# Kernel optimization log

Hardware: AMD Instinct MI355X
Metric: run time of the kernel (lower is better)

The kernel has to match this reference:

```python
import jax, jax.numpy as jnp
import numpy as np
import math

B, T, D, H = 4, 2048, 1024, 16
HD = D // H  # 64

def setup_inputs() -> dict:
    key = jax.random.key(0)
    ks = jax.random.split(key, 11)
    s = 1.0 / math.sqrt(D)
    return {
        "q": jax.random.normal(ks[0], (B, T, D), jnp.float32),
        "k": jax.random.normal(ks[1], (B, T, D), jnp.float32),
        "v": jax.random.normal(ks[2], (B, T, D), jnp.float32),
        "Wq": jax.random.normal(ks[3], (D, D), jnp.float32) * s,
        "bq": jnp.zeros((D,), jnp.float32),
        "Wk": jax.random.normal(ks[4], (D, D), jnp.float32) * s,
        "bk": jnp.zeros((D,), jnp.float32),
        "Wv": jax.random.normal(ks[5], (D, D), jnp.float32) * s,
        "bv": jnp.zeros((D,), jnp.float32),
        "Wo": jax.random.normal(ks[6], (D, D), jnp.float32) * s,
        "bo": jnp.zeros((D,), jnp.float32),
    }

def reference(q, k, v, Wq, bq, Wk, bk, Wv, bv, Wo, bo):
    # Linear projections (torch Linear: x @ W.T + b)
    qp = q @ Wq.T + bq
    kp = k @ Wk.T + bk
    vp = v @ Wv.T + bv
    # [B, T, D] -> [B, H, T, HD]
    def split(x):
        return x.reshape(B, T, H, HD).transpose(0, 2, 1, 3)
    qh, kh, vh = split(qp), split(kp), split(vp)
    # scaled dot-product attention
    score = jnp.einsum('bhqd,bhkd->bhqk', qh, kh) / math.sqrt(HD)
    attn = jax.nn.softmax(score, axis=-1)
    out = jnp.einsum('bhqk,bhkd->bhqd', attn, vh)
    # merge heads and output projection
    out = out.transpose(0, 2, 1, 3).reshape(B, T, D)
    return out @ Wo.T + bo
```

## Files before the change

kernel.cpp:

```cpp
#include <hip/hip_runtime.h>
#include <hip/hip_bf16.h>
#include <stdint.h>

#define B_ 4
#define T_ 2048
#define D_ 1024
#define H_ 16
#define HD_ 64
#define NKT (T_ / 64)

typedef __bf16 bf16;
typedef __bf16 bf16x8 __attribute__((ext_vector_type(8)));
typedef __bf16 bf16x4 __attribute__((ext_vector_type(4)));
typedef float f32x4 __attribute__((ext_vector_type(4)));
typedef uint32_t u32x4 __attribute__((ext_vector_type(4)));

#define QSCALE 0.18033688011112042f

__device__ __forceinline__ float fast_exp2(float x) {
#if __has_builtin(__builtin_amdgcn_exp2f)
    return __builtin_amdgcn_exp2f(x);
#else
    return exp2f(x);
#endif
}

__device__ __forceinline__ void async_load16(const bf16* g, const bf16* lds_uniform) {
    __builtin_amdgcn_global_load_lds(
        (const __attribute__((address_space(1))) uint32_t*)(uintptr_t)g,
        (__attribute__((address_space(3))) uint32_t*)(uintptr_t)lds_uniform,
        16, 0, 0);
}

__device__ __forceinline__ uint32_t pack2_bf16(float lo, float hi) {
    union { uint32_t u; __bf16 h[2]; } r;
    r.h[0] = (__bf16)lo;
    r.h[1] = (__bf16)hi;
    return r.u;
}

__device__ __forceinline__ void permswap16(uint32_t& a, uint32_t& b) {
    asm("v_permlane16_swap_b32 %0, %1" : "+v"(a), "+v"(b));
}

__global__ __launch_bounds__(256) void cast3(const float* __restrict__ s0, bf16* __restrict__ d0,
                                             const float* __restrict__ s1, bf16* __restrict__ d1,
                                             const float* __restrict__ s2, bf16* __restrict__ d2,
                                             int n4) {
    const float* s = blockIdx.y == 0 ? s0 : (blockIdx.y == 1 ? s1 : s2);
    bf16* d = blockIdx.y == 0 ? d0 : (blockIdx.y == 1 ? d1 : d2);
    int i = blockIdx.x * 256 + threadIdx.x;
    if (i < n4) {
        f32x4 v = ((const f32x4*)s)[i];
        bf16x4 o;
        o.x = (bf16)v.x; o.y = (bf16)v.y; o.z = (bf16)v.z; o.w = (bf16)v.w;
        ((bf16x4*)d)[i] = o;
    }
}

__global__ __launch_bounds__(256) void cast4(const float* __restrict__ s0, bf16* __restrict__ d0,
                                             const float* __restrict__ s1, bf16* __restrict__ d1,
                                             const float* __restrict__ s2, bf16* __restrict__ d2,
                                             const float* __restrict__ s3, bf16* __restrict__ d3,
                                             int n4) {
    const float* s = blockIdx.y == 0 ? s0 : (blockIdx.y == 1 ? s1 : (blockIdx.y == 2 ? s2 : s3));
    bf16* d = blockIdx.y == 0 ? d0 : (blockIdx.y == 1 ? d1 : (blockIdx.y == 2 ? d2 : d3));
    int i = blockIdx.x * 256 + threadIdx.x;
    if (i < n4) {
        f32x4 v = ((const f32x4*)s)[i];
        bf16x4 o;
        o.x = (bf16)v.x; o.y = (bf16)v.y; o.z = (bf16)v.z; o.w = (bf16)v.w;
        ((bf16x4*)d)[i] = o;
    }
}

template <typename OutT, int VMODE>
__device__ __forceinline__ void gemm_body(const bf16* __restrict__ A,
                                          const bf16* __restrict__ W,
                                          const float* __restrict__ bias,
                                          OutT* __restrict__ C,
                                          int lin, float scale,
                                          bf16* As, bf16* Bs, bf16* Tt) {
    const int K = D_, N = D_;
    const int tid = threadIdx.x;
    const int wid = tid >> 6, lane = tid & 63;
    const int quad = lane >> 4, l15 = lane & 15;
    const int wm = (wid >> 1) * 64, wn = (wid & 1) * 64;
    const int bx = N >> 7;
    const int ty = (lin & 7) + 8 * (lin / (8 * bx));
    const int tx = (lin >> 3) % bx;
    const long rowA0 = (long)ty * 128;
    const long rowB0 = (long)tx * 128;
    const int srow = lane >> 2;
    const int schunk = (lane & 3) * 8;
    const int sbase = (wid * 32) * 32;

    f32x4 acc[4][4];
#pragma unroll
    for (int i = 0; i < 4; i++)
#pragma unroll
        for (int j = 0; j < 4; j++) acc[i][j] = (f32x4){0.f, 0.f, 0.f, 0.f};

#pragma unroll
    for (int s = 0; s < 2; s++) {
        int r = wid * 32 + s * 16 + srow;
        async_load16(&A[(rowA0 + r) * K + schunk], &As[sbase + s * 16 * 32]);
        async_load16(&W[(rowB0 + r) * K + schunk], &Bs[sbase + s * 16 * 32]);
    }
    __syncthreads();

    const int NIT = K >> 5;
    for (int it = 0; it < NIT; it++) {
        const int cur = it & 1;
        const int co = cur * (128 * 32);
        if (it + 1 < NIT) {
            const int k1 = (it + 1) << 5;
            const int no = (cur ^ 1) * (128 * 32);
#pragma unroll
            for (int s = 0; s < 2; s++) {
                int r = wid * 32 + s * 16 + srow;
                async_load16(&A[(rowA0 + r) * K + k1 + schunk], &As[no + sbase + s * 16 * 32]);
                async_load16(&W[(rowB0 + r) * K + k1 + schunk], &Bs[no + sbase + s * 16 * 32]);
            }
        }
        bf16x8 af[4], bfr[4];
#pragma unroll
        for (int i = 0; i < 4; i++)
            af[i] = *(const bf16x8*)&As[co + (wm + i * 16 + l15) * 32 + quad * 8];
#pragma unroll
        for (int j = 0; j < 4; j++)
            bfr[j] = *(const bf16x8*)&Bs[co + (wn + j * 16 + l15) * 32 + quad * 8];
#pragma unroll
        for (int i = 0; i < 4; i++)
#pragma unroll
            for (int j = 0; j < 4; j++)
                acc[i][j] = __builtin_amdgcn_mfma_f32_16x16x32_bf16(af[i], bfr[j],
                                                                    acc[i][j], 0, 0, 0);
        __syncthreads();
    }

    if constexpr (VMODE == 0) {
#pragma unroll
        for (int i = 0; i < 4; i++) {
            long m = rowA0 + wm + i * 16 + quad * 4;
#pragma unroll
            for (int j = 0; j < 4; j++) {
                long n = rowB0 + wn + j * 16 + l15;
                float bb = bias[n];
#pragma unroll
                for (int r = 0; r < 4; r++) {
                    float v = (acc[i][j][r] + bb) * scale;
                    C[(m + r) * N + n] = (OutT)v;
                }
            }
        }
    } else {
#pragma unroll
        for (int i = 0; i < 4; i++) {
            int ml = wm + i * 16 + quad * 4;
#pragma unroll
            for (int j = 0; j < 4; j++) {
                int nl = wn + j * 16 + l15;
                float bb = bias[rowB0 + nl];
                bf16x4 ov = {(bf16)(acc[i][j][0] + bb), (bf16)(acc[i][j][1] + bb),
                             (bf16)(acc[i][j][2] + bb), (bf16)(acc[i][j][3] + bb)};
                *(bf16x4*)&Tt[nl * 136 + ml] = ov;
            }
        }
        __syncthreads();
        const long bidx = rowA0 >> 11;
        const int t0 = (int)(rowA0 & 2047);
#pragma unroll
        for (int p = 0; p < 8; p++) {
            int nl = p * 16 + (tid >> 4);
            int c = tid & 15;
            bf16x8 val = *(const bf16x8*)&Tt[nl * 136 + c * 8];
            int n = (int)rowB0 + nl;
            long vrow = (bidx * H_ + (n >> 6)) * (long)HD_ + (n & 63);
            int cp = (c & ~3) | ((c & 1) << 1) | ((c & 2) >> 1);
            *(bf16x8*)&((bf16*)C)[vrow * T_ + t0 + cp * 8] = val;
        }
    }
}

__global__ __launch_bounds__(256) void gemm_qkv(const bf16* __restrict__ Xq,
                                                const bf16* __restrict__ WqB,
                                                const float* __restrict__ bq,
                                                bf16* __restrict__ Qp,
                                                const bf16* __restrict__ Xk,
                                                const bf16* __restrict__ WkB,
                                                const float* __restrict__ bk,
                                                bf16* __restrict__ Kp,
                                                const bf16* __restrict__ Xv,
                                                const bf16* __restrict__ WvB,
                                                const float* __restrict__ bv,
                                                bf16* __restrict__ VtG) {
    __shared__ __align__(16) char sm[34816];
    bf16* As = (bf16*)sm;
    bf16* Bs = (bf16*)(sm + 16384);
    bf16* Tt = (bf16*)sm;
    const int p = blockIdx.x >> 9;
    const int lin = blockIdx.x & 511;
    if (p == 0)
        gemm_body<bf16, 0>(Xq, WqB, bq, Qp, lin, QSCALE, As, Bs, Tt);
    else if (p == 1)
        gemm_body<bf16, 0>(Xk, WkB, bk, Kp, lin, 1.f, As, Bs, Tt);
    else
        gemm_body<bf16, 1>(Xv, WvB, bv, VtG, lin, 1.f, As, Bs, Tt);
}

__global__ __launch_bounds__(256) void gemm_out(const bf16* __restrict__ Op,
                                                const bf16* __restrict__ WoB,
                                                const float* __restrict__ bo,
                                                float* __restrict__ out) {
    __shared__ __align__(16) char sm[32768];
    bf16* As = (bf16*)sm;
    bf16* Bs = (bf16*)(sm + 16384);
    gemm_body<float, 0>(Op, WoB, bo, out, blockIdx.x, 1.f, As, Bs, nullptr);
}

__global__ __launch_bounds__(512, 8) void attn_kernel(const bf16* __restrict__ Qp,
                                                      const bf16* __restrict__ Kp,
                                                      const bf16* __restrict__ VT,
                                                      bf16* __restrict__ Op) {
    __shared__ bf16 smem[4][64 * 64];
    const int tid = threadIdx.x;
    const int wid = tid >> 6, lane = tid & 63;
    const int quad = lane >> 4, l15 = lane & 15;
    const int q7 = l15 & 7;
    const int lin = blockIdx.x;
    const int bh = (lin & 7) + 8 * (lin >> 7);
    const int qt = (lin >> 3) & 15;
    const int b = bh >> 4, h = bh & 15;
    const long tok0 = (long)b * T_ + (long)qt * 128 + wid * 16;
    const int hcol = h * HD_;
    const long vrow0 = ((long)bh) * HD_;
    const int g_sw = ((lane & 7) ^ (lane >> 3)) * 8;
    const int srow = lane >> 3;
    const int sbase = (wid * 8) * 64;

    {
        const long krow0 = (long)b * T_;
        const int r = wid * 8 + srow;
        async_load16(&Kp[(krow0 + r) * D_ + hcol + g_sw], &smem[0][sbase]);
        async_load16(&VT[(vrow0 + r) * T_ + g_sw], &smem[2][sbase]);
    }

    bf16x8 bq0 = *(const bf16x8*)&Qp[(tok0 + l15) * D_ + hcol + quad * 8];
    bf16x8 bq1 = *(const bf16x8*)&Qp[(tok0 + l15) * D_ + hcol + 32 + quad * 8];

    const u32x4 onesu = {0x3F803F80u, 0x3F803F80u, 0x3F803F80u, 0x3F803F80u};
    const bf16x8 ones = __builtin_bit_cast(bf16x8, onesu);

    f32x4 o[4];
#pragma unroll
    for (int mt = 0; mt < 4; mt++) o[mt] = (f32x4){0.f, 0.f, 0.f, 0.f};
    f32x4 ls = (f32x4){0.f, 0.f, 0.f, 0.f};

    __syncthreads();

    for (int kt = 0; kt < NKT; kt++) {
        const int cur = kt & 1;
        if (kt + 1 < NKT) {
            const long krow1 = (long)b * T_ + (long)(kt + 1) * 64;
            const int nb = cur ^ 1;
            const int r = wid * 8 + srow;
            async_load16(&Kp[(krow1 + r) * D_ + hcol + g_sw], &smem[nb][sbase]);
            async_load16(&VT[(vrow0 + r) * T_ + (long)(kt + 1) * 64 + g_sw],
                         &smem[2 + nb][sbase]);
        }
        const bf16* Ksc = smem[cur];
        const bf16* Vsc = smem[2 + cur];

        bf16x8 pb0;
        {
            uint32_t pA[2], pB[2];
#pragma unroll
            for (int mt = 0; mt < 2; mt++) {
                bf16x8 ak0 = *(const bf16x8*)&Ksc[(mt * 16 + l15) * 64 + ((quad ^ q7) * 8)];
                bf16x8 ak1 = *(const bf16x8*)&Ksc[(mt * 16 + l15) * 64 + (((4 + quad) ^ q7) * 8)];
                f32x4 s = {0.f, 0.f, 0.f, 0.f};
                s = __builtin_amdgcn_mfma_f32_16x16x32_bf16(ak0, bq0, s, 0, 0, 0);
                s = __builtin_amdgcn_mfma_f32_16x16x32_bf16(ak1, bq1, s, 0, 0, 0);
                float p0 = fast_exp2(s[0]), p1 = fast_exp2(s[1]);
                float p2 = fast_exp2(s[2]), p3 = fast_exp2(s[3]);
                pA[mt] = pack2_bf16(p0, p1);
                pB[mt] = pack2_bf16(p2, p3);
            }
            permswap16(pA[0], pA[1]);
            permswap16(pB[0], pB[1]);
            u32x4 f = {pA[0], pB[0], pA[1], pB[1]};
            pb0 = __builtin_bit_cast(bf16x8, f);
        }
        __builtin_amdgcn_s_setprio(1);
        ls = __builtin_amdgcn_mfma_f32_16x16x32_bf16(ones, pb0, ls, 0, 0, 0);
#pragma unroll
        for (int mt = 0; mt < 4; mt++) {
            bf16x8 av0 = *(const bf16x8*)&Vsc[(mt * 16 + l15) * 64 + ((quad ^ q7) * 8)];
            o[mt] = __builtin_amdgcn_mfma_f32_16x16x32_bf16(av0, pb0, o[mt], 0, 0, 0);
        }
        __builtin_amdgcn_s_setprio(0);
        bf16x8 pb1;
        {
            uint32_t pA[2], pB[2];
#pragma unroll
            for (int mt = 0; mt < 2; mt++) {
                bf16x8 ak0 = *(const bf16x8*)&Ksc[((2 + mt) * 16 + l15) * 64 + ((quad ^ q7) * 8)];
                bf16x8 ak1 = *(const bf16x8*)&Ksc[((2 + mt) * 16 + l15) * 64 +
                                                  (((4 + quad) ^ q7) * 8)];
                f32x4 s = {0.f, 0.f, 0.f, 0.f};
                s = __builtin_amdgcn_mfma_f32_16x16x32_bf16(ak0, bq0, s, 0, 0, 0);
                s = __builtin_amdgcn_mfma_f32_16x16x32_bf16(ak1, bq1, s, 0, 0, 0);
                float p0 = fast_exp2(s[0]), p1 = fast_exp2(s[1]);
                float p2 = fast_exp2(s[2]), p3 = fast_exp2(s[3]);
                pA[mt] = pack2_bf16(p0, p1);
                pB[mt] = pack2_bf16(p2, p3);
            }
            permswap16(pA[0], pA[1]);
            permswap16(pB[0], pB[1]);
            u32x4 f = {pA[0], pB[0], pA[1], pB[1]};
            pb1 = __builtin_bit_cast(bf16x8, f);
        }
        __builtin_amdgcn_s_setprio(1);
        ls = __builtin_amdgcn_mfma_f32_16x16x32_bf16(ones, pb1, ls, 0, 0, 0);
#pragma unroll
        for (int mt = 0; mt < 4; mt++) {
            bf16x8 av1 = *(const bf16x8*)&Vsc[(mt * 16 + l15) * 64 + (((4 + quad) ^ q7) * 8)];
            o[mt] = __builtin_amdgcn_mfma_f32_16x16x32_bf16(av1, pb1, o[mt], 0, 0, 0);
        }
        __builtin_amdgcn_s_setprio(0);
        __syncthreads();
    }

    const float linv = 1.f / ls[0];

    bf16* ew = (bf16*)smem + wid * (16 * 64);
#pragma unroll
    for (int mt = 0; mt < 4; mt++) {
        bf16x4 ov = {(bf16)(o[mt][0] * linv), (bf16)(o[mt][1] * linv),
                     (bf16)(o[mt][2] * linv), (bf16)(o[mt][3] * linv)};
        *(bf16x4*)&ew[l15 * 64 + (((mt * 2 + (quad >> 1)) ^ q7) * 8) + (quad & 1) * 4] = ov;
    }
#pragma unroll
    for (int p2 = 0; p2 < 2; p2++) {
        int q = p2 * 8 + (lane >> 3);
        int dc = lane & 7;
        bf16x8 ov = *(const bf16x8*)&ew[q * 64 + ((dc ^ (q & 7)) * 8)];
        *(bf16x8*)&Op[(tok0 + q) * D_ + hcol + dc * 8] = ov;
    }
}

extern "C" void kernel_launch(void* const* d_in, const int* in_sizes, int n_in,
                              void* d_out, int out_size, void* d_ws, size_t ws_size,
                              hipStream_t stream) {
    const float* q  = (const float*)d_in[0];
    const float* k  = (const float*)d_in[1];
    const float* v  = (const float*)d_in[2];
    const float* Wq = (const float*)d_in[3];
    const float* bq = (const float*)d_in[4];
    const float* Wk = (const float*)d_in[5];
    const float* bk = (const float*)d_in[6];
    const float* Wv = (const float*)d_in[7];
    const float* bv = (const float*)d_in[8];
    const float* Wo = (const float*)d_in[9];
    const float* bo = (const float*)d_in[10];
    float* out = (float*)d_out;

    const size_t MD = (size_t)B_ * T_ * D_;
    const size_t DD = (size_t)D_ * D_;
    char* ws = (char*)d_ws;
    bf16* Xq  = (bf16*)ws; ws += MD * 2;
    bf16* Xk  = (bf16*)ws; ws += MD * 2;
    bf16* Xv  = (bf16*)ws; ws += MD * 2;
    bf16* WqB = (bf16*)ws; ws += DD * 2;
    bf16* WkB = (bf16*)ws; ws += DD * 2;
    bf16* WvB = (bf16*)ws; ws += DD * 2;
    bf16* WoB = (bf16*)ws; ws += DD * 2;
    bf16* Qp  = (bf16*)ws; ws += MD * 2;
    bf16* Kp  = (bf16*)ws; ws += MD * 2;
    bf16* VtG = (bf16*)ws; ws += MD * 2;
    bf16* Op  = (bf16*)ws; ws += MD * 2;

    cast3<<<dim3(MD / 4 / 256, 3), 256, 0, stream>>>(q, Xq, k, Xk, v, Xv, MD / 4);
    cast4<<<dim3(DD / 4 / 256, 4), 256, 0, stream>>>(Wq, WqB, Wk, WkB, Wv, WvB, Wo, WoB, DD / 4);

    gemm_qkv<<<3 * 512, 256, 0, stream>>>(Xq, WqB, bq, Qp, Xk, WkB, bk, Kp, Xv, WvB, bv, VtG);

    attn_kernel<<<B_ * H_ * (T_ / 128), 512, 0, stream>>>(Qp, Kp, VtG, Op);

    gemm_out<<<512, 256, 0, stream>>>(Op, WoB, bo, out);
}
```

Baseline: 339.1 us.

## Merge cast kernels, split V-transpose epilogue, stagger attention half-steps per wave

```diff
diff --git a/kernel.cpp b/kernel.cpp
--- a/kernel.cpp
+++ b/kernel.cpp
@@ -43,35 +43,31 @@
     asm("v_permlane16_swap_b32 %0, %1" : "+v"(a), "+v"(b));
 }
 
-__global__ __launch_bounds__(256) void cast3(const float* __restrict__ s0, bf16* __restrict__ d0,
-                                             const float* __restrict__ s1, bf16* __restrict__ d1,
-                                             const float* __restrict__ s2, bf16* __restrict__ d2,
-                                             int n4) {
-    const float* s = blockIdx.y == 0 ? s0 : (blockIdx.y == 1 ? s1 : s2);
-    bf16* d = blockIdx.y == 0 ? d0 : (blockIdx.y == 1 ? d1 : d2);
-    int i = blockIdx.x * 256 + threadIdx.x;
-    if (i < n4) {
-        f32x4 v = ((const f32x4*)s)[i];
-        bf16x4 o;
-        o.x = (bf16)v.x; o.y = (bf16)v.y; o.z = (bf16)v.z; o.w = (bf16)v.w;
-        ((bf16x4*)d)[i] = o;
-    }
-}
-
-__global__ __launch_bounds__(256) void cast4(const float* __restrict__ s0, bf16* __restrict__ d0,
-                                             const float* __restrict__ s1, bf16* __restrict__ d1,
-                                             const float* __restrict__ s2, bf16* __restrict__ d2,
-                                             const float* __restrict__ s3, bf16* __restrict__ d3,
-                                             int n4) {
-    const float* s = blockIdx.y == 0 ? s0 : (blockIdx.y == 1 ? s1 : (blockIdx.y == 2 ? s2 : s3));
-    bf16* d = blockIdx.y == 0 ? d0 : (blockIdx.y == 1 ? d1 : (blockIdx.y == 2 ? d2 : d3));
-    int i = blockIdx.x * 256 + threadIdx.x;
-    if (i < n4) {
-        f32x4 v = ((const f32x4*)s)[i];
-        bf16x4 o;
-        o.x = (bf16)v.x; o.y = (bf16)v.y; o.z = (bf16)v.z; o.w = (bf16)v.w;
-        ((bf16x4*)d)[i] = o;
-    }
+__global__ __launch_bounds__(256) void cast_all(const float* __restrict__ q, bf16* __restrict__ dq,
+                                                const float* __restrict__ k, bf16* __restrict__ dk,
+                                                const float* __restrict__ v, bf16* __restrict__ dv,
+                                                const float* __restrict__ w0, bf16* __restrict__ e0,
+                                                const float* __restrict__ w1, bf16* __restrict__ e1,
+                                                const float* __restrict__ w2, bf16* __restrict__ e2,
+                                                const float* __restrict__ w3, bf16* __restrict__ e3) {
+    long i = blockIdx.x * 256 + threadIdx.x;
+    const float* s;
+    bf16* d;
+    if (blockIdx.y < 3) {
+        s = blockIdx.y == 0 ? q : (blockIdx.y == 1 ? k : v);
+        d = blockIdx.y == 0 ? dq : (blockIdx.y == 1 ? dk : dv);
+    } else {
+        const long per = (long)(D_ * D_) / 4;
+        long wsel = i / per;
+        if (wsel >= 4) return;
+        i -= wsel * per;
+        s = wsel == 0 ? w0 : (wsel == 1 ? w1 : (wsel == 2 ? w2 : w3));
+        d = wsel == 0 ? e0 : (wsel == 1 ? e1 : (wsel == 2 ? e2 : e3));
+    }
+    f32x4 val = ((const f32x4*)s)[i];
+    bf16x4 o;
+    o.x = (bf16)val.x; o.y = (bf16)val.y; o.z = (bf16)val.z; o.w = (bf16)val.w;
+    ((bf16x4*)d)[i] = o;
 }
 
 template <typename OutT, int VMODE>
@@ -155,30 +151,36 @@
             }
         }
     } else {
-#pragma unroll
-        for (int i = 0; i < 4; i++) {
-            int ml = wm + i * 16 + quad * 4;
-#pragma unroll
-            for (int j = 0; j < 4; j++) {
-                int nl = wn + j * 16 + l15;
-                float bb = bias[rowB0 + nl];
-                bf16x4 ov = {(bf16)(acc[i][j][0] + bb), (bf16)(acc[i][j][1] + bb),
-                             (bf16)(acc[i][j][2] + bb), (bf16)(acc[i][j][3] + bb)};
-                *(bf16x4*)&Tt[nl * 136 + ml] = ov;
-            }
-        }
-        __syncthreads();
         const long bidx = rowA0 >> 11;
         const int t0 = (int)(rowA0 & 2047);
 #pragma unroll
-        for (int p = 0; p < 8; p++) {
-            int nl = p * 16 + (tid >> 4);
-            int c = tid & 15;
-            bf16x8 val = *(const bf16x8*)&Tt[nl * 136 + c * 8];
-            int n = (int)rowB0 + nl;
-            long vrow = (bidx * H_ + (n >> 6)) * (long)HD_ + (n & 63);
-            int cp = (c & ~3) | ((c & 1) << 1) | ((c & 2) >> 1);
-            *(bf16x8*)&((bf16*)C)[vrow * T_ + t0 + cp * 8] = val;
+        for (int p2 = 0; p2 < 2; p2++) {
+            if (p2) __syncthreads();
+#pragma unroll
+            for (int j2 = 0; j2 < 2; j2++) {
+                int j = p2 * 2 + j2;
+                int nl = wn + j * 16 + l15;
+                int rr = (nl & 31) + ((nl >> 6) << 5);
+                float bb = bias[rowB0 + nl];
+#pragma unroll
+                for (int i = 0; i < 4; i++) {
+                    int ml = wm + i * 16 + quad * 4;
+                    bf16x4 ov = {(bf16)(acc[i][j][0] + bb), (bf16)(acc[i][j][1] + bb),
+                                 (bf16)(acc[i][j][2] + bb), (bf16)(acc[i][j][3] + bb)};
+                    *(bf16x4*)&Tt[rr * 136 + ml] = ov;
+                }
+            }
+            __syncthreads();
+#pragma unroll
+            for (int p = 0; p < 4; p++) {
+                int idx = p * 16 + (tid >> 4);
+                int c = tid & 15;
+                bf16x8 val = *(const bf16x8*)&Tt[idx * 136 + c * 8];
+                int n = (int)rowB0 + (idx & 31) + p2 * 32 + ((idx >> 5) << 6);
+                long vrow = (bidx * H_ + (n >> 6)) * (long)HD_ + (n & 63);
+                int cp = (c & ~3) | ((c & 1) << 1) | ((c & 2) >> 1);
+                *(bf16x8*)&((bf16*)C)[vrow * T_ + t0 + cp * 8] = val;
+            }
         }
     }
 }
@@ -195,7 +197,7 @@
                                                 const bf16* __restrict__ WvB,
                                                 const float* __restrict__ bv,
                                                 bf16* __restrict__ VtG) {
-    __shared__ __align__(16) char sm[34816];
+    __shared__ __align__(16) char sm[32768];
     bf16* As = (bf16*)sm;
     bf16* Bs = (bf16*)(sm + 16384);
     bf16* Tt = (bf16*)sm;
@@ -259,6 +261,8 @@
 
     __syncthreads();
 
+    const int h0 = wid & 1;
+
     for (int kt = 0; kt < NKT; kt++) {
         const int cur = kt & 1;
         if (kt + 1 < NKT) {
@@ -272,13 +276,13 @@
         const bf16* Ksc = smem[cur];
         const bf16* Vsc = smem[2 + cur];
 
-        bf16x8 pb0;
-        {
+        auto half_step = [&](int hh) {
             uint32_t pA[2], pB[2];
 #pragma unroll
             for (int mt = 0; mt < 2; mt++) {
-                bf16x8 ak0 = *(const bf16x8*)&Ksc[(mt * 16 + l15) * 64 + ((quad ^ q7) * 8)];
-                bf16x8 ak1 = *(const bf16x8*)&Ksc[(mt * 16 + l15) * 64 + (((4 + quad) ^ q7) * 8)];
+                const bf16* kr = &Ksc[(hh * 32 + mt * 16 + l15) * 64];
+                bf16x8 ak0 = *(const bf16x8*)&kr[(quad ^ q7) * 8];
+                bf16x8 ak1 = *(const bf16x8*)&kr[((4 + quad) ^ q7) * 8];
                 f32x4 s = {0.f, 0.f, 0.f, 0.f};
                 s = __builtin_amdgcn_mfma_f32_16x16x32_bf16(ak0, bq0, s, 0, 0, 0);
                 s = __builtin_amdgcn_mfma_f32_16x16x32_bf16(ak1, bq1, s, 0, 0, 0);
@@ -290,45 +294,17 @@
             permswap16(pA[0], pA[1]);
             permswap16(pB[0], pB[1]);
             u32x4 f = {pA[0], pB[0], pA[1], pB[1]};
-            pb0 = __builtin_bit_cast(bf16x8, f);
-        }
-        __builtin_amdgcn_s_setprio(1);
-        ls = __builtin_amdgcn_mfma_f32_16x16x32_bf16(ones, pb0, ls, 0, 0, 0);
-#pragma unroll
-        for (int mt = 0; mt < 4; mt++) {
-            bf16x8 av0 = *(const bf16x8*)&Vsc[(mt * 16 + l15) * 64 + ((quad ^ q7) * 8)];
-            o[mt] = __builtin_amdgcn_mfma_f32_16x16x32_bf16(av0, pb0, o[mt], 0, 0, 0);
-        }
-        __builtin_amdgcn_s_setprio(0);
-        bf16x8 pb1;
-        {
-            uint32_t pA[2], pB[2];
-#pragma unroll
-            for (int mt = 0; mt < 2; mt++) {
-                bf16x8 ak0 = *(const bf16x8*)&Ksc[((2 + mt) * 16 + l15) * 64 + ((quad ^ q7) * 8)];
-                bf16x8 ak1 = *(const bf16x8*)&Ksc[((2 + mt) * 16 + l15) * 64 +
-                                                  (((4 + quad) ^ q7) * 8)];
-                f32x4 s = {0.f, 0.f, 0.f, 0.f};
-                s = __builtin_amdgcn_mfma_f32_16x16x32_bf16(ak0, bq0, s, 0, 0, 0);
-                s = __builtin_amdgcn_mfma_f32_16x16x32_bf16(ak1, bq1, s, 0, 0, 0);
-                float p0 = fast_exp2(s[0]), p1 = fast_exp2(s[1]);
-                float p2 = fast_exp2(s[2]), p3 = fast_exp2(s[3]);
-                pA[mt] = pack2_bf16(p0, p1);
-                pB[mt] = pack2_bf16(p2, p3);
-            }
-            permswap16(pA[0], pA[1]);
-            permswap16(pB[0], pB[1]);
-            u32x4 f = {pA[0], pB[0], pA[1], pB[1]};
-            pb1 = __builtin_bit_cast(bf16x8, f);
-        }
-        __builtin_amdgcn_s_setprio(1);
-        ls = __builtin_amdgcn_mfma_f32_16x16x32_bf16(ones, pb1, ls, 0, 0, 0);
-#pragma unroll
-        for (int mt = 0; mt < 4; mt++) {
-            bf16x8 av1 = *(const bf16x8*)&Vsc[(mt * 16 + l15) * 64 + (((4 + quad) ^ q7) * 8)];
-            o[mt] = __builtin_amdgcn_mfma_f32_16x16x32_bf16(av1, pb1, o[mt], 0, 0, 0);
-        }
-        __builtin_amdgcn_s_setprio(0);
+            bf16x8 pb = __builtin_bit_cast(bf16x8, f);
+            ls = __builtin_amdgcn_mfma_f32_16x16x32_bf16(ones, pb, ls, 0, 0, 0);
+            const int vch = ((hh * 4 + quad) ^ q7) * 8;
+#pragma unroll
+            for (int mt = 0; mt < 4; mt++) {
+                bf16x8 av = *(const bf16x8*)&Vsc[(mt * 16 + l15) * 64 + vch];
+                o[mt] = __builtin_amdgcn_mfma_f32_16x16x32_bf16(av, pb, o[mt], 0, 0, 0);
+            }
+        };
+        half_step(h0);
+        half_step(h0 ^ 1);
         __syncthreads();
     }
 
@@ -381,8 +357,8 @@
     bf16* VtG = (bf16*)ws; ws += MD * 2;
     bf16* Op  = (bf16*)ws; ws += MD * 2;
 
-    cast3<<<dim3(MD / 4 / 256, 3), 256, 0, stream>>>(q, Xq, k, Xk, v, Xv, MD / 4);
-    cast4<<<dim3(DD / 4 / 256, 4), 256, 0, stream>>>(Wq, WqB, Wk, WkB, Wv, WvB, Wo, WoB, DD / 4);
+    cast_all<<<dim3(MD / 4 / 256, 4), 256, 0, stream>>>(q, Xq, k, Xk, v, Xv,
+                                                        Wq, WqB, Wk, WkB, Wv, WvB, Wo, WoB);
 
     gemm_qkv<<<3 * 512, 256, 0, stream>>>(Xq, WqB, bq, Qp, Xk, WkB, bk, Kp, Xv, WvB, bv, VtG);
 
```

New measurement: 336.6 us. About the same (-0.7%).
